# Optimization experiments

Hardware: AMD Instinct MI355X
Metric: run time of the kernel (lower is better)

The kernel has to match this reference:

```python
import jax, jax.numpy as jnp
import numpy as np
import math

B, S, D = 4, 2048, 1024
H, DH = 16, 64  # num_heads, head dim (hardcoded 64 in module)


def setup_inputs() -> dict:
    key = jax.random.key(0)
    ks = jax.random.split(key, 5)
    scale = 0.02
    return {
        "x": jax.random.normal(ks[0], (B, S, D), dtype=jnp.float32),
        "W_Q": jax.random.normal(ks[1], (D, H * DH), dtype=jnp.float32) * scale,
        "W_K": jax.random.normal(ks[2], (D, H * DH), dtype=jnp.float32) * scale,
        "W_V": jax.random.normal(ks[3], (D, H * DH), dtype=jnp.float32) * scale,
        "W_O": jax.random.normal(ks[4], (H * DH, D), dtype=jnp.float32) * scale,
        "ln_gamma": jnp.ones((D,), dtype=jnp.float32),
        "ln_beta": jnp.zeros((D,), dtype=jnp.float32),
    }


def reference(x, W_Q, W_K, W_V, W_O, ln_gamma, ln_beta):
    # QKV projections (bias=False Linear: x @ W)
    q = (x @ W_Q).reshape(B, S, H, DH).transpose(0, 2, 1, 3)  # [B,H,S,DH]
    k = (x @ W_K).reshape(B, S, H, DH).transpose(0, 2, 1, 3)
    v = (x @ W_V).reshape(B, S, H, DH).transpose(0, 2, 1, 3)

    # scaled scores with causal mask (upper triangle, diag=1 -> -1e7)
    scores = jnp.einsum("bhsd,bhtd->bhst", q, k) / math.sqrt(DH)  # [B,H,S,S]
    causal = jnp.triu(jnp.ones((S, S), dtype=bool), k=1)
    scores = jnp.where(causal, jnp.float32(-1e7), scores)
    attn = jax.nn.softmax(scores, axis=-1)
    ctx = jnp.einsum("bhst,bhtd->bhsd", attn, v)  # [B,H,S,DH]

    # merge heads, output proj, residual, LayerNorm
    out = ctx.transpose(0, 2, 1, 3).reshape(B, S, H * DH) @ W_O + x
    mu = jnp.mean(out, axis=-1, keepdims=True)
    var = jnp.mean((out - mu) ** 2, axis=-1, keepdims=True)
    out = (out - mu) * jax.lax.rsqrt(var + 1e-5) * ln_gamma + ln_beta
    return out
```

## Files before the change

kernel.cpp:

```cpp
#include <hip/hip_runtime.h>
#include <hip/hip_bf16.h>
#include <cstdint>
#include <cstddef>

#define S_ 2048
#define D_ 1024
#define H_ 16
#define DH_ 64
#define M_ 8192

using bf16 = __bf16;
using bf16x4 = __attribute__((ext_vector_type(4))) __bf16;
using bf16x8 = __attribute__((ext_vector_type(8))) __bf16;
using f32x4 = __attribute__((ext_vector_type(4))) float;
using s16x4 = __attribute__((ext_vector_type(4))) short;

__device__ __forceinline__ void g2lds16(const bf16* g, bf16* l) {
  __builtin_amdgcn_global_load_lds(
      (const __attribute__((address_space(1))) void*)g,
      (__attribute__((address_space(3))) void*)l, 16, 0, 0);
}

__device__ __forceinline__ f32x4 mfma16(bf16x4 a, bf16x4 b, f32x4 c) {
#if __has_builtin(__builtin_amdgcn_mfma_f32_16x16x16_bf16)
  return __builtin_amdgcn_mfma_f32_16x16x16_bf16(a, b, c, 0, 0, 0);
#elif __has_builtin(__builtin_amdgcn_mfma_f32_16x16x16bf16_1k)
  return __builtin_amdgcn_mfma_f32_16x16x16bf16_1k(
      __builtin_bit_cast(s16x4, a), __builtin_bit_cast(s16x4, b), c, 0, 0, 0);
#else
  f32x4 d;
  asm("v_mfma_f32_16x16x16_bf16 %0, %1, %2, %3"
      : "=v"(d)
      : "v"(a), "v"(b), "v"(c));
  return d;
#endif
}

__global__ __launch_bounds__(256) void cvt_all_kernel(
    const float* __restrict__ x, const float* __restrict__ w0,
    const float* __restrict__ w1, const float* __restrict__ w2,
    const float* __restrict__ w3, bf16* __restrict__ xb,
    bf16* __restrict__ o0, bf16* __restrict__ o1, bf16* __restrict__ o2,
    bf16* __restrict__ o3) {
  __shared__ float tile[32][33];
  int bx = blockIdx.x;
  int tid = threadIdx.x;
  if (bx < 4096) {
    size_t i = ((size_t)bx * 256 + tid) * 8;
    float4 a = *(const float4*)(x + i);
    float4 b = *(const float4*)(x + i + 4);
    bf16x8 o;
    o[0] = (bf16)a.x; o[1] = (bf16)a.y; o[2] = (bf16)a.z; o[3] = (bf16)a.w;
    o[4] = (bf16)b.x; o[5] = (bf16)b.y; o[6] = (bf16)b.z; o[7] = (bf16)b.w;
    *(bf16x8*)(xb + i) = o;
    return;
  }
  int wb = bx - 4096;
  int wsel = wb >> 10; wb &= 1023;
  const float* W; bf16* O;
  switch (wsel) {
    case 0: W = w0; O = o0; break;
    case 1: W = w1; O = o1; break;
    case 2: W = w2; O = o2; break;
    default: W = w3; O = o3; break;
  }
  int n0 = (wb & 31) * 32;
  int k0 = (wb >> 5) * 32;
#pragma unroll
  for (int i = 0; i < 4; ++i) {
    int e = tid + i * 256; int rr = e >> 5, cc = e & 31;
    tile[rr][cc] = W[(size_t)(k0 + rr) * 1024 + n0 + cc];
  }
  __syncthreads();
#pragma unroll
  for (int i = 0; i < 4; ++i) {
    int e = tid + i * 256; int rr = e >> 5, cc = e & 31;
    O[(size_t)(n0 + rr) * 1024 + k0 + cc] = (bf16)tile[cc][rr];
  }
}

template <int MODE>
__global__ __launch_bounds__(512, 2) void gemm_kernel(
    const bf16* __restrict__ A,
    const bf16* __restrict__ Bt0, const bf16* __restrict__ Bt1,
    const bf16* __restrict__ Bt2,
    bf16* __restrict__ Qo, bf16* __restrict__ Ko, bf16* __restrict__ Vto,
    const float* __restrict__ xres, float* __restrict__ out) {
  extern __shared__ float4 smem4[];
  bf16* smem = (bf16*)smem4;

  constexpr int NWG = (MODE == 0) ? 768 : 256;
  constexpr int CPX = NWG / 8;
  constexpr int NBN = (MODE == 0) ? 12 : 4;
  const int wg = ((int)blockIdx.x & 7) * CPX + ((int)blockIdx.x >> 3);
  const int bn = wg % NBN, bm = wg / NBN;

  const bf16* Bt;
  int n0full = 0, wsel = 0;
  if constexpr (MODE == 0) {
    wsel = bn >> 2;
    Bt = (wsel == 0) ? Bt0 : (wsel == 1 ? Bt1 : Bt2);
    n0full = (bn & 3) * 256;
  } else {
    Bt = Bt0;
    n0full = bn * 256;
  }

  const int tid = threadIdx.x;
  const int wave = tid >> 6, lane = tid & 63;
  const int quad = lane >> 4, r = lane & 15;
  const int wm = (wave >> 2) * 64, wn = (wave & 3) * 64;

  const int lrow = lane >> 3;
  const int lcol = ((lane & 7) ^ lrow) * 8;
  const int am0 = bm * 128 + wave * 8 + lrow;
  const int am1 = am0 + 64;
  const bf16 *p0, *p1, *p2, *p3, *p4, *p5;
  if constexpr (MODE == 0) {
    p0 = A + (size_t)am0 * 1024 + lcol;
    p1 = A + (size_t)am1 * 1024 + lcol;
  } else {
    p0 = A + (size_t)(am0 >> 11) * (16 * (size_t)S_ * DH_) +
         (size_t)(am0 & 2047) * 64 + lcol;
    p1 = A + (size_t)(am1 >> 11) * (16 * (size_t)S_ * DH_) +
         (size_t)(am1 & 2047) * 64 + lcol;
  }
  const int bnr = n0full + wave * 8 + lrow;
  p2 = Bt + (size_t)bnr * 1024 + lcol;
  p3 = Bt + (size_t)(bnr + 64) * 1024 + lcol;
  p4 = Bt + (size_t)(bnr + 128) * 1024 + lcol;
  p5 = Bt + (size_t)(bnr + 192) * 1024 + lcol;
  constexpr ptrdiff_t dA = (MODE == 0) ? 64 : (ptrdiff_t)S_ * DH_;

  const int oA0 = wave * 512, oA1 = (8 + wave) * 512;
  const int oB0 = 8192 + wave * 512, oB1 = 8192 + (8 + wave) * 512;
  const int oB2 = 8192 + (16 + wave) * 512, oB3 = 8192 + (24 + wave) * 512;

  auto stage = [&](bf16* base) {
    g2lds16(p0, base + oA0); p0 += dA;
    g2lds16(p1, base + oA1); p1 += dA;
    g2lds16(p2, base + oB0); p2 += 64;
    g2lds16(p3, base + oB1); p3 += 64;
    g2lds16(p4, base + oB2); p4 += 64;
    g2lds16(p5, base + oB3); p5 += 64;
  };

  f32x4 acc[4][4];
  const f32x4 zero = {0.f, 0.f, 0.f, 0.f};
#pragma unroll
  for (int i = 0; i < 4; ++i)
#pragma unroll
    for (int j = 0; j < 4; ++j) acc[i][j] = zero;

  const int rw = r & 7;
  const int x0 = (quad ^ rw) * 8;
  const int x1 = ((quad + 4) ^ rw) * 8;
  const int raB = (wm + r) * 64;
  const int rbB = (wn + r) * 64;

  auto phases = [&](const bf16* buf) {
    const bf16* bA = buf;
    const bf16* bB = buf + 8192;
    bf16x8 af[4], bg[4];
#pragma unroll
    for (int i = 0; i < 4; ++i)
      af[i] = *(const bf16x8*)(bA + raB + i * 1024 + x0);
#pragma unroll
    for (int j = 0; j < 4; ++j)
      bg[j] = *(const bf16x8*)(bB + rbB + j * 1024 + x0);
    __builtin_amdgcn_s_setprio(1);
#pragma unroll
    for (int i = 0; i < 4; ++i)
#pragma unroll
      for (int j = 0; j < 4; ++j)
        acc[i][j] = __builtin_amdgcn_mfma_f32_16x16x32_bf16(af[i], bg[j],
                                                            acc[i][j], 0, 0, 0);
    __builtin_amdgcn_s_setprio(0);
    asm volatile("s_barrier" ::: "memory");
#pragma unroll
    for (int i = 0; i < 4; ++i)
      af[i] = *(const bf16x8*)(bA + raB + i * 1024 + x1);
#pragma unroll
    for (int j = 0; j < 4; ++j)
      bg[j] = *(const bf16x8*)(bB + rbB + j * 1024 + x1);
    __builtin_amdgcn_s_setprio(1);
#pragma unroll
    for (int i = 0; i < 4; ++i)
#pragma unroll
      for (int j = 0; j < 4; ++j)
        acc[i][j] = __builtin_amdgcn_mfma_f32_16x16x32_bf16(af[i], bg[j],
                                                            acc[i][j], 0, 0, 0);
    __builtin_amdgcn_s_setprio(0);
  };

  bf16* b0 = smem;
  bf16* b1 = smem + 24576;
  bf16* b2 = smem + 49152;

  stage(b0);
  stage(b1);

#pragma unroll 1
  for (int kt = 0; kt < 15; kt += 3) {
    asm volatile("s_waitcnt vmcnt(6)\n\ts_barrier" ::: "memory");
    stage(b2);
    phases(b0);
    asm volatile("s_waitcnt vmcnt(6)\n\ts_barrier" ::: "memory");
    stage(b0);
    phases(b1);
    asm volatile("s_waitcnt vmcnt(6)\n\ts_barrier" ::: "memory");
    if (kt < 12) stage(b1);
    phases(b2);
  }
  asm volatile("s_waitcnt vmcnt(0)\n\ts_barrier" ::: "memory");
  phases(b0);

  const int mB = bm * 128 + wm + quad * 4;
  if constexpr (MODE == 0) {
    if (wsel < 2) {
      bf16* dst = (wsel == 0) ? Qo : Ko;
#pragma unroll
      for (int i = 0; i < 4; ++i) {
#pragma unroll
        for (int j = 0; j < 4; ++j) {
          int n = n0full + wn + j * 16 + r;
          int h = n >> 6, dh = n & 63;
#pragma unroll
          for (int g = 0; g < 4; ++g) {
            int m = mB + i * 16 + g;
            int b = m >> 11, s = m & 2047;
            dst[((size_t)(b * H_ + h) * S_ + s) * DH_ + dh] =
                (bf16)acc[i][j][g];
          }
        }
      }
    } else {
#pragma unroll
      for (int i = 0; i < 4; ++i) {
        int m = mB + i * 16;
        int b = m >> 11, s = m & 2047;
#pragma unroll
        for (int j = 0; j < 4; ++j) {
          int n = n0full + wn + j * 16 + r;
          int h = n >> 6, dh = n & 63;
          bf16x4 pk;
#pragma unroll
          for (int g = 0; g < 4; ++g) pk[g] = (bf16)acc[i][j][g];
          *(bf16x4*)(Vto + ((size_t)(b * H_ + h) * DH_ + dh) * S_ + s) = pk;
        }
      }
    }
  } else {
#pragma unroll
    for (int i = 0; i < 4; ++i) {
#pragma unroll
      for (int j = 0; j < 4; ++j) {
        int n = bn * 256 + wn + j * 16 + r;
#pragma unroll
        for (int g = 0; g < 4; ++g) {
          int m = mB + i * 16 + g;
          size_t idx = (size_t)m * 1024 + n;
          out[idx] = acc[i][j][g] + xres[idx];
        }
      }
    }
  }
}

__global__ __launch_bounds__(256) void attn_kernel(const bf16* __restrict__ Qb,
                                                   const bf16* __restrict__ Kb,
                                                   const bf16* __restrict__ Vtb,
                                                   bf16* __restrict__ ctx) {
  __shared__ __align__(16) bf16 smK[2][64 * 64];
  __shared__ __align__(16) bf16 smV[2][64 * 64];
  const int bh = blockIdx.x & 63, p = blockIdx.x >> 6;
  const bf16* Qh = Qb + (size_t)bh * S_ * DH_;
  const bf16* Kh = Kb + (size_t)bh * S_ * DH_;
  const bf16* Vh = Vtb + (size_t)bh * DH_ * S_;
  bf16* Ch = ctx + (size_t)bh * S_ * DH_;
  const int tid = threadIdx.x, wave = tid >> 6, lane = tid & 63;
  const int quad = lane >> 4, r = lane & 15;
  const int r7 = r & 7;
  const int c0 = 2 * wave, c1 = c0 + 1;
  const int sr = lane >> 3;
  const int gcol = ((lane & 7) ^ (sr & 7)) * 8;
  const f32x4 zero = {0.f, 0.f, 0.f, 0.f};
  const int xk0 = (quad ^ r7) * 8, xk1 = ((quad + 4) ^ r7) * 8;

  for (int ph = 0; ph < 2; ++ph) {
    const int i128 = ph ? (15 - p) : p;
    const int qB = i128 * 128;
    const int q0w = qB + wave * 32;
    const int numkt = 2 * i128 + 2;

    bf16x8 qf[2][2];
    const float qsc = 0.125f * 1.44269504f;
#pragma unroll
    for (int qg = 0; qg < 2; ++qg)
#pragma unroll
      for (int hh = 0; hh < 2; ++hh) {
        bf16x8 q = *(const bf16x8*)(Qh + (size_t)(q0w + qg * 16 + r) * DH_ +
                                    hh * 32 + quad * 8);
#pragma unroll
        for (int i = 0; i < 8; ++i) q[i] = (bf16)((float)q[i] * qsc);
        qf[qg][hh] = q;
      }

    f32x4 lacc[2] = {zero, zero};
    f32x4 oacc[2][4];
#pragma unroll
    for (int qg = 0; qg < 2; ++qg)
#pragma unroll
      for (int tn = 0; tn < 4; ++tn) oacc[qg][tn] = zero;

    g2lds16(Kh + (size_t)(c0 * 8 + sr) * DH_ + gcol, &smK[0][c0 * 512]);
    g2lds16(Kh + (size_t)(c1 * 8 + sr) * DH_ + gcol, &smK[0][c1 * 512]);
    g2lds16(Vh + (size_t)(c0 * 8 + sr) * S_ + gcol, &smV[0][c0 * 512]);
    g2lds16(Vh + (size_t)(c1 * 8 + sr) * S_ + gcol, &smV[0][c1 * 512]);

    for (int kt = 0; kt < numkt; ++kt) {
      const int cur = kt & 1;
      const int kv0 = kt * 64;
      if (kt + 1 < numkt) {
        const int nk = kv0 + 64;
        g2lds16(Kh + (size_t)(nk + c0 * 8 + sr) * DH_ + gcol, &smK[1 - cur][c0 * 512]);
        g2lds16(Kh + (size_t)(nk + c1 * 8 + sr) * DH_ + gcol, &smK[1 - cur][c1 * 512]);
        g2lds16(Vh + (size_t)(c0 * 8 + sr) * S_ + nk + gcol, &smV[1 - cur][c0 * 512]);
        g2lds16(Vh + (size_t)(c1 * 8 + sr) * S_ + nk + gcol, &smV[1 - cur][c1 * 512]);
        asm volatile("s_waitcnt vmcnt(4)\n\ts_barrier" ::: "memory");
      } else {
        asm volatile("s_waitcnt vmcnt(0)\n\ts_barrier" ::: "memory");
      }
      if (kv0 <= q0w + 31) {
        const bf16* kb = &smK[cur][0];
        const bf16* vb = &smV[cur][0];

        f32x4 s[2][4];
#pragma unroll
        for (int t = 0; t < 4; ++t) {
          bf16x8 kf0 = *(const bf16x8*)(kb + (t * 16 + r) * 64 + xk0);
          bf16x8 kf1 = *(const bf16x8*)(kb + (t * 16 + r) * 64 + xk1);
#pragma unroll
          for (int qg = 0; qg < 2; ++qg) {
            f32x4 z = __builtin_amdgcn_mfma_f32_16x16x32_bf16(kf0, qf[qg][0],
                                                              zero, 0, 0, 0);
            s[qg][t] = __builtin_amdgcn_mfma_f32_16x16x32_bf16(kf1, qf[qg][1],
                                                               z, 0, 0, 0);
          }
        }
        if (kt >= numkt - 2) {
#pragma unroll
          for (int qg = 0; qg < 2; ++qg) {
            const int q = q0w + qg * 16 + r;
#pragma unroll
            for (int t = 0; t < 4; ++t) {
              const int kv = kv0 + t * 16 + quad * 4;
#pragma unroll
              for (int g = 0; g < 4; ++g)
                if (kv + g > q) s[qg][t][g] = -1e30f;
            }
          }
        }
#pragma unroll
        for (int t = 0; t < 4; ++t) {
          bf16x4 pa[2];
#pragma unroll
          for (int qg = 0; qg < 2; ++qg) {
#pragma unroll
            for (int g = 0; g < 4; ++g)
              s[qg][t][g] = __builtin_amdgcn_exp2f(s[qg][t][g]);
            lacc[qg] += s[qg][t];
            bf16x4 pk;
#pragma unroll
            for (int g = 0; g < 4; ++g) pk[g] = (bf16)s[qg][t][g];
            pa[qg] = pk;
          }
#pragma unroll
          for (int tn = 0; tn < 4; ++tn) {
            bf16x4 vf = *(const bf16x4*)(
                vb + (tn * 16 + r) * 64 +
                ((2 * t + (quad >> 1)) ^ r7) * 8 + (quad & 1) * 4);
            oacc[0][tn] = mfma16(pa[0], vf, oacc[0][tn]);
            oacc[1][tn] = mfma16(pa[1], vf, oacc[1][tn]);
          }
        }
      }
      asm volatile("s_waitcnt lgkmcnt(0)\n\ts_barrier" ::: "memory");
    }

#pragma unroll
    for (int qg = 0; qg < 2; ++qg) {
      float rs = (lacc[qg][0] + lacc[qg][1]) + (lacc[qg][2] + lacc[qg][3]);
      rs += __shfl_xor(rs, 16, 64);
      rs += __shfl_xor(rs, 32, 64);
      const float inv = 1.f / rs;
      f32x4 ib;
#pragma unroll
      for (int g = 0; g < 4; ++g) ib[g] = __shfl(inv, quad * 4 + g, 64);
#pragma unroll
      for (int tn = 0; tn < 4; ++tn) {
        f32x4 ov = oacc[qg][tn] * ib;
#pragma unroll
        for (int g = 0; g < 4; ++g)
          Ch[(size_t)(q0w + qg * 16 + quad * 4 + g) * DH_ + tn * 16 + r] =
              (bf16)ov[g];
      }
    }
  }
}

__global__ __launch_bounds__(256) void ln_kernel(float* __restrict__ out,
                                                 const float* __restrict__ gamma,
                                                 const float* __restrict__ beta) {
  __shared__ float red[8];
  size_t row = blockIdx.x;
  float* p = out + row * 1024;
  int tid = threadIdx.x;
  float4 v = ((const float4*)p)[tid];
  float s1 = v.x + v.y + v.z + v.w;
  float s2 = v.x * v.x + v.y * v.y + v.z * v.z + v.w * v.w;
#pragma unroll
  for (int o = 1; o < 64; o <<= 1) {
    s1 += __shfl_xor(s1, o, 64);
    s2 += __shfl_xor(s2, o, 64);
  }
  int wave = tid >> 6, lane = tid & 63;
  if (lane == 0) { red[wave] = s1; red[4 + wave] = s2; }
  __syncthreads();
  s1 = red[0] + red[1] + red[2] + red[3];
  s2 = red[4] + red[5] + red[6] + red[7];
  float mean = s1 * (1.f / 1024.f);
  float var = s2 * (1.f / 1024.f) - mean * mean;
  float rstd = rsqrtf(var + 1e-5f);
  float4 g = ((const float4*)gamma)[tid];
  float4 b = ((const float4*)beta)[tid];
  float4 o;
  o.x = (v.x - mean) * rstd * g.x + b.x;
  o.y = (v.y - mean) * rstd * g.y + b.y;
  o.z = (v.z - mean) * rstd * g.z + b.z;
  o.w = (v.w - mean) * rstd * g.w + b.w;
  ((float4*)p)[tid] = o;
}

extern "C" void kernel_launch(void* const* d_in, const int* in_sizes, int n_in,
                              void* d_out, int out_size, void* d_ws,
                              size_t ws_size, hipStream_t stream) {
  (void)in_sizes; (void)n_in; (void)out_size; (void)ws_size;
  const float* x  = (const float*)d_in[0];
  const float* WQ = (const float*)d_in[1];
  const float* WK = (const float*)d_in[2];
  const float* WV = (const float*)d_in[3];
  const float* WO = (const float*)d_in[4];
  const float* gamma = (const float*)d_in[5];
  const float* beta  = (const float*)d_in[6];
  float* out = (float*)d_out;

  bf16* ws = (bf16*)d_ws;
  const size_t MD = (size_t)M_ * D_;
  const size_t WW = (size_t)D_ * D_;
  bf16* xb   = ws;
  bf16* wqt  = xb + MD;
  bf16* wkt  = wqt + WW;
  bf16* wvt  = wkt + WW;
  bf16* wot  = wvt + WW;
  bf16* Qb   = wot + WW;
  bf16* Kb   = Qb + MD;
  bf16* Vtb  = Kb + MD;
  bf16* ctxb = Vtb + MD;

  constexpr int GEMM_LDS = 3 * 48 * 1024;
  static bool s_attr = false;
  if (!s_attr) {
    s_attr = true;
    (void)hipFuncSetAttribute(reinterpret_cast<const void*>(gemm_kernel<0>),
                              hipFuncAttributeMaxDynamicSharedMemorySize,
                              GEMM_LDS);
    (void)hipFuncSetAttribute(reinterpret_cast<const void*>(gemm_kernel<1>),
                              hipFuncAttributeMaxDynamicSharedMemorySize,
                              GEMM_LDS);
  }

  cvt_all_kernel<<<dim3(8192), dim3(256), 0, stream>>>(
      x, WQ, WK, WV, WO, xb, wqt, wkt, wvt, wot);
  gemm_kernel<0><<<dim3(768), dim3(512), GEMM_LDS, stream>>>(
      xb, wqt, wkt, wvt, Qb, Kb, Vtb, nullptr, nullptr);
  attn_kernel<<<dim3(512), dim3(256), 0, stream>>>(Qb, Kb, Vtb, ctxb);
  gemm_kernel<1><<<dim3(256), dim3(512), GEMM_LDS, stream>>>(
      ctxb, wot, nullptr, nullptr, nullptr, nullptr, nullptr, x, out);
  ln_kernel<<<dim3(8192), dim3(256), 0, stream>>>(out, gamma, beta);
}
```

Measured before the change: 253.2 us.

## Split attention block into 8 waves of 16 query rows each

The attention kernel now launches 512 threads per block, so each of 8 waves handles 16 query rows instead of 4 waves handling 32. Each wave issues one K and one V async LDS load per tile instead of two of each, and the causal skip and mask are computed per 16-row wave. This aims to raise wave-level parallelism and cut per-wave register pressure (launch bounds 512,4). In exchange, K fragments read from LDS are reused across fewer query rows, so LDS traffic per MFMA rises and barrier participation grows.

```diff
diff --git a/kernel.cpp b/kernel.cpp
--- a/kernel.cpp
+++ b/kernel.cpp
@@ -267,10 +267,10 @@
   }
 }
 
-__global__ __launch_bounds__(256) void attn_kernel(const bf16* __restrict__ Qb,
-                                                   const bf16* __restrict__ Kb,
-                                                   const bf16* __restrict__ Vtb,
-                                                   bf16* __restrict__ ctx) {
+__global__ __launch_bounds__(512, 4) void attn_kernel(const bf16* __restrict__ Qb,
+                                                      const bf16* __restrict__ Kb,
+                                                      const bf16* __restrict__ Vtb,
+                                                      bf16* __restrict__ ctx) {
   __shared__ __align__(16) bf16 smK[2][64 * 64];
   __shared__ __align__(16) bf16 smV[2][64 * 64];
   const int bh = blockIdx.x & 63, p = blockIdx.x >> 6;
@@ -281,130 +281,104 @@
   const int tid = threadIdx.x, wave = tid >> 6, lane = tid & 63;
   const int quad = lane >> 4, r = lane & 15;
   const int r7 = r & 7;
-  const int c0 = 2 * wave, c1 = c0 + 1;
-  const int sr = lane >> 3;
-  const int gcol = ((lane & 7) ^ (sr & 7)) * 8;
+  const int wrow = wave * 8 + (lane >> 3);
+  const int gcol = ((lane & 7) ^ (lane >> 3)) * 8;
   const f32x4 zero = {0.f, 0.f, 0.f, 0.f};
   const int xk0 = (quad ^ r7) * 8, xk1 = ((quad + 4) ^ r7) * 8;
 
   for (int ph = 0; ph < 2; ++ph) {
     const int i128 = ph ? (15 - p) : p;
     const int qB = i128 * 128;
-    const int q0w = qB + wave * 32;
+    const int q0w = qB + wave * 16;
     const int numkt = 2 * i128 + 2;
-
-    bf16x8 qf[2][2];
+    const int lastkt = q0w >> 6;
+
+    bf16x8 qf[2];
     const float qsc = 0.125f * 1.44269504f;
 #pragma unroll
-    for (int qg = 0; qg < 2; ++qg)
-#pragma unroll
-      for (int hh = 0; hh < 2; ++hh) {
-        bf16x8 q = *(const bf16x8*)(Qh + (size_t)(q0w + qg * 16 + r) * DH_ +
-                                    hh * 32 + quad * 8);
-#pragma unroll
-        for (int i = 0; i < 8; ++i) q[i] = (bf16)((float)q[i] * qsc);
-        qf[qg][hh] = q;
-      }
-
-    f32x4 lacc[2] = {zero, zero};
-    f32x4 oacc[2][4];
-#pragma unroll
-    for (int qg = 0; qg < 2; ++qg)
-#pragma unroll
-      for (int tn = 0; tn < 4; ++tn) oacc[qg][tn] = zero;
-
-    g2lds16(Kh + (size_t)(c0 * 8 + sr) * DH_ + gcol, &smK[0][c0 * 512]);
-    g2lds16(Kh + (size_t)(c1 * 8 + sr) * DH_ + gcol, &smK[0][c1 * 512]);
-    g2lds16(Vh + (size_t)(c0 * 8 + sr) * S_ + gcol, &smV[0][c0 * 512]);
-    g2lds16(Vh + (size_t)(c1 * 8 + sr) * S_ + gcol, &smV[0][c1 * 512]);
+    for (int hh = 0; hh < 2; ++hh) {
+      bf16x8 q = *(const bf16x8*)(Qh + (size_t)(q0w + r) * DH_ +
+                                  hh * 32 + quad * 8);
+#pragma unroll
+      for (int i = 0; i < 8; ++i) q[i] = (bf16)((float)q[i] * qsc);
+      qf[hh] = q;
+    }
+
+    f32x4 lacc = zero;
+    f32x4 oacc[4] = {zero, zero, zero, zero};
+
+    g2lds16(Kh + (size_t)wrow * DH_ + gcol, &smK[0][wave * 512]);
+    g2lds16(Vh + (size_t)wrow * S_ + gcol, &smV[0][wave * 512]);
 
     for (int kt = 0; kt < numkt; ++kt) {
       const int cur = kt & 1;
       const int kv0 = kt * 64;
       if (kt + 1 < numkt) {
         const int nk = kv0 + 64;
-        g2lds16(Kh + (size_t)(nk + c0 * 8 + sr) * DH_ + gcol, &smK[1 - cur][c0 * 512]);
-        g2lds16(Kh + (size_t)(nk + c1 * 8 + sr) * DH_ + gcol, &smK[1 - cur][c1 * 512]);
-        g2lds16(Vh + (size_t)(c0 * 8 + sr) * S_ + nk + gcol, &smV[1 - cur][c0 * 512]);
-        g2lds16(Vh + (size_t)(c1 * 8 + sr) * S_ + nk + gcol, &smV[1 - cur][c1 * 512]);
-        asm volatile("s_waitcnt vmcnt(4)\n\ts_barrier" ::: "memory");
+        g2lds16(Kh + (size_t)(nk + wrow) * DH_ + gcol, &smK[1 - cur][wave * 512]);
+        g2lds16(Vh + (size_t)wrow * S_ + nk + gcol, &smV[1 - cur][wave * 512]);
+        asm volatile("s_waitcnt vmcnt(2)\n\ts_barrier" ::: "memory");
       } else {
         asm volatile("s_waitcnt vmcnt(0)\n\ts_barrier" ::: "memory");
       }
-      if (kv0 <= q0w + 31) {
+      if (kt <= lastkt) {
         const bf16* kb = &smK[cur][0];
         const bf16* vb = &smV[cur][0];
 
-        f32x4 s[2][4];
+        f32x4 s[4];
 #pragma unroll
         for (int t = 0; t < 4; ++t) {
           bf16x8 kf0 = *(const bf16x8*)(kb + (t * 16 + r) * 64 + xk0);
           bf16x8 kf1 = *(const bf16x8*)(kb + (t * 16 + r) * 64 + xk1);
-#pragma unroll
-          for (int qg = 0; qg < 2; ++qg) {
-            f32x4 z = __builtin_amdgcn_mfma_f32_16x16x32_bf16(kf0, qf[qg][0],
-                                                              zero, 0, 0, 0);
-            s[qg][t] = __builtin_amdgcn_mfma_f32_16x16x32_bf16(kf1, qf[qg][1],
-                                                               z, 0, 0, 0);
+          f32x4 z = __builtin_amdgcn_mfma_f32_16x16x32_bf16(kf0, qf[0],
+                                                            zero, 0, 0, 0);
+          s[t] = __builtin_amdgcn_mfma_f32_16x16x32_bf16(kf1, qf[1],
+                                                         z, 0, 0, 0);
+        }
+        if (kt == lastkt) {
+          const int q = q0w + r;
+#pragma unroll
+          for (int t = 0; t < 4; ++t) {
+            const int kv = kv0 + t * 16 + quad * 4;
+#pragma unroll
+            for (int g = 0; g < 4; ++g)
+              if (kv + g > q) s[t][g] = -1e30f;
           }
         }
-        if (kt >= numkt - 2) {
-#pragma unroll
-          for (int qg = 0; qg < 2; ++qg) {
-            const int q = q0w + qg * 16 + r;
-#pragma unroll
-            for (int t = 0; t < 4; ++t) {
-              const int kv = kv0 + t * 16 + quad * 4;
-#pragma unroll
-              for (int g = 0; g < 4; ++g)
-                if (kv + g > q) s[qg][t][g] = -1e30f;
-            }
-          }
-        }
 #pragma unroll
         for (int t = 0; t < 4; ++t) {
-          bf16x4 pa[2];
-#pragma unroll
-          for (int qg = 0; qg < 2; ++qg) {
-#pragma unroll
-            for (int g = 0; g < 4; ++g)
-              s[qg][t][g] = __builtin_amdgcn_exp2f(s[qg][t][g]);
-            lacc[qg] += s[qg][t];
-            bf16x4 pk;
-#pragma unroll
-            for (int g = 0; g < 4; ++g) pk[g] = (bf16)s[qg][t][g];
-            pa[qg] = pk;
-          }
+#pragma unroll
+          for (int g = 0; g < 4; ++g)
+            s[t][g] = __builtin_amdgcn_exp2f(s[t][g]);
+          lacc += s[t];
+          bf16x4 pa;
+#pragma unroll
+          for (int g = 0; g < 4; ++g) pa[g] = (bf16)s[t][g];
 #pragma unroll
           for (int tn = 0; tn < 4; ++tn) {
             bf16x4 vf = *(const bf16x4*)(
                 vb + (tn * 16 + r) * 64 +
                 ((2 * t + (quad >> 1)) ^ r7) * 8 + (quad & 1) * 4);
-            oacc[0][tn] = mfma16(pa[0], vf, oacc[0][tn]);
-            oacc[1][tn] = mfma16(pa[1], vf, oacc[1][tn]);
+            oacc[tn] = mfma16(pa, vf, oacc[tn]);
           }
         }
       }
       asm volatile("s_waitcnt lgkmcnt(0)\n\ts_barrier" ::: "memory");
     }
 
-#pragma unroll
-    for (int qg = 0; qg < 2; ++qg) {
-      float rs = (lacc[qg][0] + lacc[qg][1]) + (lacc[qg][2] + lacc[qg][3]);
-      rs += __shfl_xor(rs, 16, 64);
-      rs += __shfl_xor(rs, 32, 64);
-      const float inv = 1.f / rs;
-      f32x4 ib;
-#pragma unroll
-      for (int g = 0; g < 4; ++g) ib[g] = __shfl(inv, quad * 4 + g, 64);
-#pragma unroll
-      for (int tn = 0; tn < 4; ++tn) {
-        f32x4 ov = oacc[qg][tn] * ib;
-#pragma unroll
-        for (int g = 0; g < 4; ++g)
-          Ch[(size_t)(q0w + qg * 16 + quad * 4 + g) * DH_ + tn * 16 + r] =
-              (bf16)ov[g];
-      }
+    float rs = (lacc[0] + lacc[1]) + (lacc[2] + lacc[3]);
+    rs += __shfl_xor(rs, 16, 64);
+    rs += __shfl_xor(rs, 32, 64);
+    const float inv = 1.f / rs;
+    f32x4 ib;
+#pragma unroll
+    for (int g = 0; g < 4; ++g) ib[g] = __shfl(inv, quad * 4 + g, 64);
+#pragma unroll
+    for (int tn = 0; tn < 4; ++tn) {
+      f32x4 ov = oacc[tn] * ib;
+#pragma unroll
+      for (int g = 0; g < 4; ++g)
+        Ch[(size_t)(q0w + quad * 4 + g) * DH_ + tn * 16 + r] = (bf16)ov[g];
     }
   }
 }
@@ -484,7 +458,7 @@
       x, WQ, WK, WV, WO, xb, wqt, wkt, wvt, wot);
   gemm_kernel<0><<<dim3(768), dim3(512), GEMM_LDS, stream>>>(
       xb, wqt, wkt, wvt, Qb, Kb, Vtb, nullptr, nullptr);
-  attn_kernel<<<dim3(512), dim3(256), 0, stream>>>(Qb, Kb, Vtb, ctxb);
+  attn_kernel<<<dim3(512), dim3(512), 0, stream>>>(Qb, Kb, Vtb, ctxb);
   gemm_kernel<1><<<dim3(256), dim3(512), GEMM_LDS, stream>>>(
       ctxb, wot, nullptr, nullptr, nullptr, nullptr, nullptr, x, out);
   ln_kernel<<<dim3(8192), dim3(256), 0, stream>>>(out, gamma, beta);
```

Result: no change. 254.1 us (+0.3%).

## Enlarge attention query tile to 256 rows with 8 waves per block

Applied to the files above, without the earlier changes.

The attention kernel now processes 256 query rows per block with 512 threads (8 waves), halving the grid to 256 blocks. Each staged K/V tile is shared by twice as many waves, which halves redundant global-to-LDS traffic. Each wave now loads one 16-byte chunk per tile instead of two, and the barrier now waits for all outstanding loads. The per-wave causal cutoff uses a precomputed last tile index. The cost is fewer blocks, coarser causal load balance, and more barrier contention across 8 waves, where waves that finish early still wait at every barrier.

```diff
diff --git a/kernel.cpp b/kernel.cpp
--- a/kernel.cpp
+++ b/kernel.cpp
@@ -267,31 +267,30 @@
   }
 }
 
-__global__ __launch_bounds__(256) void attn_kernel(const bf16* __restrict__ Qb,
-                                                   const bf16* __restrict__ Kb,
-                                                   const bf16* __restrict__ Vtb,
-                                                   bf16* __restrict__ ctx) {
+__global__ __launch_bounds__(512, 2) void attn_kernel(const bf16* __restrict__ Qb,
+                                                      const bf16* __restrict__ Kb,
+                                                      const bf16* __restrict__ Vtb,
+                                                      bf16* __restrict__ ctx) {
   __shared__ __align__(16) bf16 smK[2][64 * 64];
   __shared__ __align__(16) bf16 smV[2][64 * 64];
-  const int bh = blockIdx.x & 63, p = blockIdx.x >> 6;
+  const int bh = blockIdx.x & 63, pr = blockIdx.x >> 6;
   const bf16* Qh = Qb + (size_t)bh * S_ * DH_;
   const bf16* Kh = Kb + (size_t)bh * S_ * DH_;
   const bf16* Vh = Vtb + (size_t)bh * DH_ * S_;
   bf16* Ch = ctx + (size_t)bh * S_ * DH_;
   const int tid = threadIdx.x, wave = tid >> 6, lane = tid & 63;
   const int quad = lane >> 4, r = lane & 15;
-  const int r7 = r & 7;
-  const int c0 = 2 * wave, c1 = c0 + 1;
-  const int sr = lane >> 3;
-  const int gcol = ((lane & 7) ^ (sr & 7)) * 8;
+  const int r7 = r & 15 & 7;
+  const int wrow = wave * 8 + (lane >> 3);
+  const int gcol = ((lane & 7) ^ (lane >> 3)) * 8;
   const f32x4 zero = {0.f, 0.f, 0.f, 0.f};
   const int xk0 = (quad ^ r7) * 8, xk1 = ((quad + 4) ^ r7) * 8;
 
   for (int ph = 0; ph < 2; ++ph) {
-    const int i128 = ph ? (15 - p) : p;
-    const int qB = i128 * 128;
-    const int q0w = qB + wave * 32;
-    const int numkt = 2 * i128 + 2;
+    const int i256 = ph ? (7 - pr) : pr;
+    const int q0w = i256 * 256 + wave * 32;
+    const int numkt = 4 * i256 + 4;
+    const int lastkt = q0w >> 6;
 
     bf16x8 qf[2][2];
     const float qsc = 0.125f * 1.44269504f;
@@ -313,25 +312,19 @@
 #pragma unroll
       for (int tn = 0; tn < 4; ++tn) oacc[qg][tn] = zero;
 
-    g2lds16(Kh + (size_t)(c0 * 8 + sr) * DH_ + gcol, &smK[0][c0 * 512]);
-    g2lds16(Kh + (size_t)(c1 * 8 + sr) * DH_ + gcol, &smK[0][c1 * 512]);
-    g2lds16(Vh + (size_t)(c0 * 8 + sr) * S_ + gcol, &smV[0][c0 * 512]);
-    g2lds16(Vh + (size_t)(c1 * 8 + sr) * S_ + gcol, &smV[0][c1 * 512]);
+    g2lds16(Kh + (size_t)wrow * DH_ + gcol, &smK[0][wave * 512]);
+    g2lds16(Vh + (size_t)wrow * S_ + gcol, &smV[0][wave * 512]);
+    asm volatile("s_waitcnt vmcnt(0)\n\ts_barrier" ::: "memory");
 
     for (int kt = 0; kt < numkt; ++kt) {
       const int cur = kt & 1;
       const int kv0 = kt * 64;
       if (kt + 1 < numkt) {
         const int nk = kv0 + 64;
-        g2lds16(Kh + (size_t)(nk + c0 * 8 + sr) * DH_ + gcol, &smK[1 - cur][c0 * 512]);
-        g2lds16(Kh + (size_t)(nk + c1 * 8 + sr) * DH_ + gcol, &smK[1 - cur][c1 * 512]);
-        g2lds16(Vh + (size_t)(c0 * 8 + sr) * S_ + nk + gcol, &smV[1 - cur][c0 * 512]);
-        g2lds16(Vh + (size_t)(c1 * 8 + sr) * S_ + nk + gcol, &smV[1 - cur][c1 * 512]);
-        asm volatile("s_waitcnt vmcnt(4)\n\ts_barrier" ::: "memory");
-      } else {
-        asm volatile("s_waitcnt vmcnt(0)\n\ts_barrier" ::: "memory");
-      }
-      if (kv0 <= q0w + 31) {
+        g2lds16(Kh + (size_t)(nk + wrow) * DH_ + gcol, &smK[1 - cur][wave * 512]);
+        g2lds16(Vh + (size_t)wrow * S_ + nk + gcol, &smV[1 - cur][wave * 512]);
+      }
+      if (kt <= lastkt) {
         const bf16* kb = &smK[cur][0];
         const bf16* vb = &smV[cur][0];
 
@@ -348,7 +341,7 @@
                                                                z, 0, 0, 0);
           }
         }
-        if (kt >= numkt - 2) {
+        if (kt == lastkt) {
 #pragma unroll
           for (int qg = 0; qg < 2; ++qg) {
             const int q = q0w + qg * 16 + r;
@@ -385,7 +378,7 @@
           }
         }
       }
-      asm volatile("s_waitcnt lgkmcnt(0)\n\ts_barrier" ::: "memory");
+      asm volatile("s_waitcnt vmcnt(0) lgkmcnt(0)\n\ts_barrier" ::: "memory");
     }
 
 #pragma unroll
@@ -484,7 +477,7 @@
       x, WQ, WK, WV, WO, xb, wqt, wkt, wvt, wot);
   gemm_kernel<0><<<dim3(768), dim3(512), GEMM_LDS, stream>>>(
       xb, wqt, wkt, wvt, Qb, Kb, Vtb, nullptr, nullptr);
-  attn_kernel<<<dim3(512), dim3(256), 0, stream>>>(Qb, Kb, Vtb, ctxb);
+  attn_kernel<<<dim3(256), dim3(512), 0, stream>>>(Qb, Kb, Vtb, ctxb);
   gemm_kernel<1><<<dim3(256), dim3(512), GEMM_LDS, stream>>>(
       ctxb, wot, nullptr, nullptr, nullptr, nullptr, nullptr, x, out);
   ln_kernel<<<dim3(8192), dim3(256), 0, stream>>>(out, gamma, beta);
```

New measurement: 259.6 us. +2.5%, slower.
